# Kernel tuning notes

Measured on AMD Instinct MI355X. Metric: run time of the kernel, lower is better.

The kernel has to match this reference:

```python
import jax, jax.numpy as jnp
import numpy as np

EPS = 1e-5
KS = 3
PAD = 1


def _bn(x, g, b, m, v):
    inv = g / jnp.sqrt(v + EPS)
    return x * inv[None, :, None, None] + (b - m * inv)[None, :, None, None]


def _deform_conv2d(x, off_w, off_b, w):
    # x: (B,C,H,W); off_w: (2*9,C,3,3); w: (Cout,C,3,3)
    B, C, H, W = x.shape
    N = KS * KS
    off = jax.lax.conv_general_dilated(x, off_w, (1, 1), ((PAD, PAD), (PAD, PAD)))
    off = off + off_b[None, :, None, None]                      # (B,2N,H,W)
    xp = jnp.pad(x, ((0, 0), (0, 0), (PAD, PAD), (PAD, PAD)))
    Hp, Wp = H + 2 * PAD, W + 2 * PAD
    r = jnp.arange(KS, dtype=x.dtype) - (KS - 1) // 2           # kernel offsets
    pny = jnp.repeat(r, KS)                                     # row-major (dy)
    pnx = jnp.tile(r, KS)                                       # row-major (dx)
    p0y = jnp.arange(1, H + 1, dtype=x.dtype)[None, None, :, None]
    p0x = jnp.arange(1, W + 1, dtype=x.dtype)[None, None, None, :]
    py = off[:, :N] + pny[None, :, None, None] + p0y            # (B,N,H,W)
    px = off[:, N:] + pnx[None, :, None, None] + p0x
    py = jnp.clip(py, 0.0, Hp - 1.0)
    px = jnp.clip(px, 0.0, Wp - 1.0)
    fy = jax.lax.stop_gradient(jnp.floor(py))                   # indices detached (as in torch impl)
    fx = jax.lax.stop_gradient(jnp.floor(px))
    qy0 = jnp.clip(fy, 0.0, Hp - 1.0)
    qx0 = jnp.clip(fx, 0.0, Wp - 1.0)
    qy1 = jnp.clip(fy + 1.0, 0.0, Hp - 1.0)
    qx1 = jnp.clip(fx + 1.0, 0.0, Wp - 1.0)
    xf = xp.reshape(B, C, Hp * Wp)

    def gather(qy, qx):
        idx = (qy * Wp + qx).astype(jnp.int32)                  # (B,N,H,W)
        return jax.vmap(lambda m_, i_: m_[:, i_])(xf, idx)       # (B,C,N,H,W)

    g_lt = (1.0 + (qy0 - py)) * (1.0 + (qx0 - px))
    g_rb = (1.0 - (qy1 - py)) * (1.0 - (qx1 - px))
    g_lb = (1.0 + (qy0 - py)) * (1.0 - (qx1 - px))
    g_rt = (1.0 - (qy1 - py)) * (1.0 + (qx0 - px))
    xo = (g_lt[:, None] * gather(qy0, qx0) + g_rb[:, None] * gather(qy1, qx1)
          + g_lb[:, None] * gather(qy0, qx1) + g_rt[:, None] * gather(qy1, qx0))
    # (B,C,N,H,W) -> (B,C,H*KS,W*KS): N = (row, col) row-major
    xo = xo.reshape(B, C, KS, KS, H, W).transpose(0, 1, 4, 2, 5, 3).reshape(B, C, H * KS, W * KS)
    return jax.lax.conv_general_dilated(xo, w, (KS, KS), 'VALID')


def _forward(x, dc1_offw, dc1_offb, dc1_w, bn1_g, bn1_b, bn1_m, bn1_v,
             dc2_offw, dc2_offb, dc2_w, bn2_g, bn2_b, bn2_m, bn2_v,
             id_w, id_b, bn3_g, bn3_b, bn3_m, bn3_v):
    h = jax.nn.relu(_bn(_deform_conv2d(x, dc1_offw, dc1_offb, dc1_w), bn1_g, bn1_b, bn1_m, bn1_v))
    h = _bn(_deform_conv2d(h, dc2_offw, dc2_offb, dc2_w), bn2_g, bn2_b, bn2_m, bn2_v)
    idt = jnp.einsum('bchw,oc->bohw', x, id_w[:, :, 0, 0]) + id_b[None, :, None, None]
    idt = _bn(idt, bn3_g, bn3_b, bn3_m, bn3_v)
    return jax.nn.relu(h + idt)


def setup_inputs() -> dict:
    key = jax.random.key(0)
    ks = jax.random.split(key, 16)
    B, Cin, Cout, H, W = 2, 64, 128, 128, 128
    N2 = 2 * KS * KS
    d = {}
    d['x'] = jax.random.normal(ks[0], (B, Cin, H, W), jnp.float32)
    d['dc1_offw'] = jax.random.normal(ks[1], (N2, Cin, KS, KS), jnp.float32) * 0.01
    d['dc1_offb'] = jnp.zeros((N2,), jnp.float32)
    d['dc1_w'] = jax.random.normal(ks[2], (Cout, Cin, KS, KS), jnp.float32) * 0.05
    d['bn1_g'] = 1.0 + 0.1 * jax.random.normal(ks[3], (Cout,), jnp.float32)
    d['bn1_b'] = 0.1 * jax.random.normal(ks[4], (Cout,), jnp.float32)
    d['bn1_m'] = 0.1 * jax.random.normal(ks[5], (Cout,), jnp.float32)
    d['bn1_v'] = jnp.ones((Cout,), jnp.float32)
    d['dc2_offw'] = jax.random.normal(ks[6], (N2, Cout, KS, KS), jnp.float32) * 0.01
    d['dc2_offb'] = jnp.zeros((N2,), jnp.float32)
    d['dc2_w'] = jax.random.normal(ks[7], (Cout, Cout, KS, KS), jnp.float32) * 0.03
    d['bn2_g'] = 1.0 + 0.1 * jax.random.normal(ks[8], (Cout,), jnp.float32)
    d['bn2_b'] = 0.1 * jax.random.normal(ks[9], (Cout,), jnp.float32)
    d['bn2_m'] = 0.1 * jax.random.normal(ks[10], (Cout,), jnp.float32)
    d['bn2_v'] = jnp.ones((Cout,), jnp.float32)
    d['id_w'] = jax.random.normal(ks[11], (Cout, Cin, 1, 1), jnp.float32) * 0.1
    d['id_b'] = jnp.zeros((Cout,), jnp.float32)
    d['bn3_g'] = 1.0 + 0.1 * jax.random.normal(ks[12], (Cout,), jnp.float32)
    d['bn3_b'] = 0.1 * jax.random.normal(ks[13], (Cout,), jnp.float32)
    d['bn3_m'] = 0.1 * jax.random.normal(ks[14], (Cout,), jnp.float32)
    d['bn3_v'] = jnp.ones((Cout,), jnp.float32)
    return d


def reference(x, dc1_offw, dc1_offb, dc1_w, bn1_g, bn1_b, bn1_m, bn1_v,
              dc2_offw, dc2_offb, dc2_w, bn2_g, bn2_b, bn2_m, bn2_v,
              id_w, id_b, bn3_g, bn3_b, bn3_m, bn3_v):
    return _forward(x, dc1_offw, dc1_offb, dc1_w, bn1_g, bn1_b, bn1_m, bn1_v,
                    dc2_offw, dc2_offb, dc2_w, bn2_g, bn2_b, bn2_m, bn2_v,
                    id_w, id_b, bn3_g, bn3_b, bn3_m, bn3_v)
```

## Files before the change

kernel.cpp:

```cpp
#include <hip/hip_runtime.h>
#include <math.h>

#define HH 128
#define WW 128
#define HWSZ (HH * WW)
#define BB 2
#define COUT 128

typedef __bf16 bf16x8 __attribute__((ext_vector_type(8)));
typedef float f32x4 __attribute__((ext_vector_type(4)));
typedef float f32x2 __attribute__((ext_vector_type(2)));
typedef short s16x8 __attribute__((ext_vector_type(8)));
typedef short s16x4 __attribute__((ext_vector_type(4)));
typedef unsigned short u16x4 __attribute__((ext_vector_type(4)));
typedef unsigned short u16x8 __attribute__((ext_vector_type(8)));

__device__ __forceinline__ short tobf(float f) {
  union { float f; unsigned u; } v; v.f = f;
  unsigned r = v.u + 0x7fffu + ((v.u >> 16) & 1u);
  return (short)(r >> 16);
}
__device__ __forceinline__ float asf(unsigned u) {
  union { unsigned u; float f; } v; v.u = u;
  return v.f;
}
__device__ __forceinline__ f32x2 up2(unsigned u) {
  f32x2 r; r[0] = asf(u << 16); r[1] = asf(u & 0xffff0000u); return r;
}
__device__ __forceinline__ unsigned trunc2bf(f32x2 v) {
  union { float f; unsigned u; } a, b;
  a.f = v[0]; b.f = v[1];
  return __builtin_amdgcn_perm(b.u, a.u, 0x07060302u);
}

#define PA0 73728
#define PA1 221184
#define PA2 229376
#define PA3 247808
#define PA4 284672
#define PA5 284928
__global__ __launch_bounds__(256) void prep_all_kernel(
    const float* __restrict__ dc1_w, const float* __restrict__ dc2_w,
    const float* __restrict__ id_w, const float* __restrict__ dc1_offw,
    const float* __restrict__ dc2_offw,
    const float* g1, const float* b1, const float* m1, const float* v1,
    const float* g2, const float* b2, const float* m2, const float* v2,
    const float* g3, const float* b3, const float* m3, const float* v3,
    const float* idb,
    short* __restrict__ wbf1, short* __restrict__ wbf2,
    short* __restrict__ woff1, short* __restrict__ woff2,
    float* __restrict__ cb1, float* __restrict__ cb2) {
  int idx = blockIdx.x * 256 + threadIdx.x;
  if (idx < PA0) {
    int o = idx / 576, k = idx - o * 576;
    float inv = g1[o] / sqrtf(v1[o] + 1e-5f);
    int col = (k % 9) * 64 + k / 9;
    int di = (((col >> 5) * 2 + (o >> 6)) * 4 + ((o >> 4) & 3)) * 512
           + (((o & 15) | (((col >> 3) & 3) << 4)) * 8) + (col & 7);
    wbf1[di] = tobf(dc1_w[(size_t)o * 576 + k] * inv);
  } else if (idx < PA1) {
    int j = idx - PA0;
    int o = j / 1152, k = j - o * 1152;
    float inv = g2[o] / sqrtf(v2[o] + 1e-5f);
    int col = (k % 9) * 128 + k / 9;
    int di = (((col >> 5) * 2 + (o >> 6)) * 4 + ((o >> 4) & 3)) * 512
           + (((o & 15) | (((col >> 3) & 3) << 4)) * 8) + (col & 7);
    wbf2[di] = tobf(dc2_w[(size_t)o * 1152 + k] * inv);
  } else if (idx < PA2) {
    int j = idx - PA1;
    int o = j >> 6, k = j & 63;
    float inv = g3[o] / sqrtf(v3[o] + 1e-5f);
    int col = 1152 + k;
    int di = (((col >> 5) * 2 + (o >> 6)) * 4 + ((o >> 4) & 3)) * 512
           + (((o & 15) | (((col >> 3) & 3) << 4)) * 8) + (col & 7);
    wbf2[di] = tobf(id_w[(size_t)o * 64 + k] * inv);
  } else if (idx < PA3) {
    int j = idx - PA2;
    int o = j / 576, k = j - o * 576;
    int col = (k % 9) * 64 + k / 9;
    int di = ((col >> 5) * 2 + (o >> 4)) * 512 + ((col >> 3) & 3) * 128
           + (o & 15) * 8 + (col & 7);
    woff1[di] = (o < 18) ? tobf(dc1_offw[(size_t)o * 576 + k]) : (short)0;
  } else if (idx < PA4) {
    int j = idx - PA3;
    int o = j / 1152, k = j - o * 1152;
    int col = (k % 9) * 128 + k / 9;
    int di = ((col >> 5) * 2 + (o >> 4)) * 512 + ((col >> 3) & 3) * 128
           + (o & 15) * 8 + (col & 7);
    woff2[di] = (o < 18) ? tobf(dc2_offw[(size_t)o * 1152 + k]) : (short)0;
  } else if (idx < PA5) {
    int j = idx - PA4;
    if (j < 128) {
      float inv = g1[j] / sqrtf(v1[j] + 1e-5f);
      cb1[j] = b1[j] - m1[j] * inv;
    } else {
      int o = j - 128;
      float inv2_ = g2[o] / sqrtf(v2[o] + 1e-5f);
      float inv3_ = g3[o] / sqrtf(v3[o] + 1e-5f);
      cb2[o] = (b2[o] - m2[o] * inv2_) + idb[o] * inv3_ + (b3[o] - m3[o] * inv3_);
    }
  }
}

__global__ __launch_bounds__(256) void xcast_kernel(const float* __restrict__ x,
                                                    unsigned short* __restrict__ xn) {
  __shared__ short lds[64 * 72];
  int tid = threadIdx.x;
  int gp0 = blockIdx.x * 64;
  int b = gp0 >> 14;
  int pl0 = gp0 & 16383;
  int p = tid & 63;
  int cb = (tid >> 6) * 16;
#pragma unroll
  for (int i = 0; i < 16; i++) {
    int c = cb + i;
    lds[p * 72 + c] = tobf(x[((size_t)(b * 64 + c)) * HWSZ + pl0 + p]);
  }
  __syncthreads();
  int pw = tid >> 2, cseg = (tid & 3) * 16;
  u16x8 a = *(const u16x8*)&lds[pw * 72 + cseg];
  u16x8 b8 = *(const u16x8*)&lds[pw * 72 + cseg + 8];
  *(u16x8*)&xn[(size_t)(gp0 + pw) * 64 + cseg] = a;
  *(u16x8*)&xn[(size_t)(gp0 + pw) * 64 + cseg + 8] = b8;
}

template <int CSH>
__global__ __launch_bounds__(512, 4) void offconv_mfma_kernel(
    const unsigned short* __restrict__ in, const short* __restrict__ woff,
    const float* __restrict__ offb, float* __restrict__ off) {
  __shared__ float redf[4 * 64 * 8];
  constexpr int Cin = 1 << CSH;
  constexpr int HK = (9 << CSH) >> 1;
  constexpr int NCh = HK >> 5;
  const int tid = threadIdx.x;
  const int lane = tid & 63, wv = tid >> 6;
  const int pxg = wv & 3, kh = wv >> 2;
  const int pb = ((blockIdx.x & 7) << 6) | (blockIdx.x >> 3);
  const int pix0 = pb << 6;
  const int x0 = pix0 & 127, y = (pix0 >> 7) & 127, b = pix0 >> 14;
  const unsigned short* inb = in + (size_t)b * HWSZ * Cin;
  const int l15 = lane & 15, quad = lane >> 4;
  const int px = x0 + pxg * 16 + l15;

  f32x4 acc[2];
  acc[0] = (f32x4){0.f, 0.f, 0.f, 0.f};
  acc[1] = (f32x4){0.f, 0.f, 0.f, 0.f};

#pragma unroll
  for (int i = 0; i < NCh; i++) {
    int k0 = kh * HK + i * 32;
    int n = k0 >> CSH;
    int c0 = (k0 & (Cin - 1)) + quad * 8;
    int yy = y + n / 3 - 1;
    int xx = px + n % 3 - 1;
    bf16x8 bv = {};
    if (((unsigned)yy < (unsigned)HH) && ((unsigned)xx < (unsigned)WW))
      bv = *(const bf16x8*)&inb[((size_t)yy * WW + xx) * Cin + c0];
    int fbase = (k0 >> 5) * 1024 + lane * 8;
    bf16x8 a0 = *(const bf16x8*)&woff[fbase];
    bf16x8 a1 = *(const bf16x8*)&woff[fbase + 512];
    acc[0] = __builtin_amdgcn_mfma_f32_16x16x32_bf16(a0, bv, acc[0], 0, 0, 0);
    acc[1] = __builtin_amdgcn_mfma_f32_16x16x32_bf16(a1, bv, acc[1], 0, 0, 0);
  }
  if (kh == 1) {
    *(f32x4*)&redf[(pxg * 64 + lane) * 8] = acc[0];
    *(f32x4*)&redf[(pxg * 64 + lane) * 8 + 4] = acc[1];
  }
  __syncthreads();
  if (kh == 0) {
    acc[0] += *(const f32x4*)&redf[(pxg * 64 + lane) * 8];
    acc[1] += *(const f32x4*)&redf[(pxg * 64 + lane) * 8 + 4];
#pragma unroll
    for (int ot = 0; ot < 2; ot++) {
#pragma unroll
      for (int r = 0; r < 4; r++) {
        int o = ot * 16 + quad * 4 + r;
        if (o < 18)
          off[(size_t)(b * 18 + o) * HWSZ + y * WW + px] = acc[ot][r] + offb[o];
      }
    }
  }
}

#define LOADW(P, kc_)                                           \
  {                                                             \
    const short* wf_ = wfb + (size_t)(kc_) * 4096;              \
    P##w0 = *(const bf16x8*)(wf_);                              \
    P##w1 = *(const bf16x8*)(wf_ + 512);                        \
    P##w2 = *(const bf16x8*)(wf_ + 1024);                       \
    P##w3 = *(const bf16x8*)(wf_ + 1536);                       \
    P##w4 = *(const bf16x8*)(wf_ + 2048);                       \
    P##w5 = *(const bf16x8*)(wf_ + 2560);                       \
    P##w6 = *(const bf16x8*)(wf_ + 3072);                       \
    P##w7 = *(const bf16x8*)(wf_ + 3584);                       \
  }

#define LOADT(P, kc_)                                           \
  {                                                             \
    int k0_ = (kc_) << 5;                                       \
    int n_ = k0_ >> CSH;                                        \
    int c0_ = (k0_ & (Cin - 1)) + cq * 8;                       \
    uint4 d4_ = dsu[(n_ << 5) + dp];                            \
    int dx_ = (int)(d4_.w & 0xffffu);                           \
    int dy_ = (int)d4_.w >> 16;                                 \
    const unsigned short* ptr_ = inb + (int)d4_.z + c0_;        \
    P##q0 = *(const uint4*)(ptr_);                              \
    P##q1 = *(const uint4*)(ptr_ + dx_);                        \
    P##q2 = *(const uint4*)(ptr_ + dy_);                        \
    P##q3 = *(const uint4*)(ptr_ + dx_ + dy_);                  \
    P##wa = d4_.x;                                              \
    P##wb = d4_.y;                                              \
  }

#define COMPUTE(P)                                                            \
  {                                                                           \
    float w0_ = asf(P##wa << 16), w1_ = asf(P##wa & 0xffff0000u);             \
    float w2_ = asf(P##wb << 16), w3_ = asf(P##wb & 0xffff0000u);             \
    f32x2 v0_ = up2(P##q0.x) * w0_ + up2(P##q1.x) * w1_                       \
              + up2(P##q2.x) * w2_ + up2(P##q3.x) * w3_;                      \
    f32x2 v1_ = up2(P##q0.y) * w0_ + up2(P##q1.y) * w1_                       \
              + up2(P##q2.y) * w2_ + up2(P##q3.y) * w3_;                      \
    f32x2 v2_ = up2(P##q0.z) * w0_ + up2(P##q1.z) * w1_                       \
              + up2(P##q2.z) * w2_ + up2(P##q3.z) * w3_;                      \
    f32x2 v3_ = up2(P##q0.w) * w0_ + up2(P##q1.w) * w1_                       \
              + up2(P##q2.w) * w2_ + up2(P##q3.w) * w3_;                      \
    union { int i[4]; bf16x8 v; } bu_;                                        \
    bu_.i[0] = __builtin_amdgcn_ds_bpermute(baddr, (int)trunc2bf(v0_));       \
    bu_.i[1] = __builtin_amdgcn_ds_bpermute(baddr, (int)trunc2bf(v1_));       \
    bu_.i[2] = __builtin_amdgcn_ds_bpermute(baddr, (int)trunc2bf(v2_));       \
    bu_.i[3] = __builtin_amdgcn_ds_bpermute(baddr, (int)trunc2bf(v3_));       \
    bf16x8 bfr_ = bu_.v;                                                      \
    acc[0] = __builtin_amdgcn_mfma_f32_16x16x32_bf16(P##w0, bfr_, acc[0], 0, 0, 0); \
    acc[1] = __builtin_amdgcn_mfma_f32_16x16x32_bf16(P##w1, bfr_, acc[1], 0, 0, 0); \
    acc[2] = __builtin_amdgcn_mfma_f32_16x16x32_bf16(P##w2, bfr_, acc[2], 0, 0, 0); \
    acc[3] = __builtin_amdgcn_mfma_f32_16x16x32_bf16(P##w3, bfr_, acc[3], 0, 0, 0); \
    acc[4] = __builtin_amdgcn_mfma_f32_16x16x32_bf16(P##w4, bfr_, acc[4], 0, 0, 0); \
    acc[5] = __builtin_amdgcn_mfma_f32_16x16x32_bf16(P##w5, bfr_, acc[5], 0, 0, 0); \
    acc[6] = __builtin_amdgcn_mfma_f32_16x16x32_bf16(P##w6, bfr_, acc[6], 0, 0, 0); \
    acc[7] = __builtin_amdgcn_mfma_f32_16x16x32_bf16(P##w7, bfr_, acc[7], 0, 0, 0); \
  }

template <int CSH, int KCONV, int KTOT, int MODE>
__global__ __launch_bounds__(256, 3) void deform_mfma_kernel(
    const unsigned short* __restrict__ in, const float* __restrict__ off,
    const short* __restrict__ wbf, const float* __restrict__ cbv,
    const unsigned short* __restrict__ xid, float* __restrict__ outf,
    unsigned short* __restrict__ outb) {
  __shared__ __align__(16) char smem[25088];
  uint4* dsu = (uint4*)smem;
  f32x4* redf = (f32x4*)smem;
  short* trans = (short*)(smem + 16384);

  const int tid = threadIdx.x;
  const int lane = tid & 63, wv = tid >> 6;
  const int pb = ((blockIdx.x & 7) << 7) | (blockIdx.x >> 3);
  const int pix0 = pb << 5;
  const int x0 = pix0 & 127, y = (pix0 >> 7) & 127, b = pix0 >> 14;
  constexpr int Cin = 1 << CSH;
  const unsigned short* inb = in + (size_t)b * HWSZ * Cin;
  const int l15 = lane & 15, quad = lane >> 4;
  const int pxg = wv & 1, kh = wv >> 1;
  const int dp = pxg * 16 + (lane >> 2);
  const int cq = lane & 3;
  const int baddr = (((lane & 15) << 2) | (lane >> 4)) << 2;

  constexpr int NC = KTOT >> 5;
  constexpr int NCONV = KCONV >> 5;
  constexpr int HC = NC >> 1;
  const int kcBeg = kh * HC;
  const int kcEnd = kcBeg + HC;
  const int kcEndConv = (kcEnd < NCONV) ? kcEnd : NCONV;
  const short* wfb = wbf + lane * 8;

  bf16x8 Aw0, Aw1, Aw2, Aw3, Aw4, Aw5, Aw6, Aw7;
  bf16x8 Bw0, Bw1, Bw2, Bw3, Bw4, Bw5, Bw6, Bw7;
  uint4 Aq0, Aq1, Aq2, Aq3, Bq0, Bq1, Bq2, Bq3;
  unsigned Awa, Awb, Bwa, Bwb;

  LOADW(A, kcBeg);

  for (int t = tid; t < 288; t += 256) {
    int n = t >> 5, pp = t & 31;
    float offy = off[(size_t)(b * 18 + n) * HWSZ + y * WW + x0 + pp];
    float offx = off[(size_t)(b * 18 + 9 + n) * HWSZ + y * WW + x0 + pp];
    float py = offy + (float)(n / 3 - 1) + (float)(y + 1);
    float px = offx + (float)(n % 3 - 1) + (float)(x0 + pp + 1);
    py = fminf(fmaxf(py, 0.f), 129.f);
    px = fminf(fmaxf(px, 0.f), 129.f);
    float fy = floorf(py), fx = floorf(px);
    float qy1 = fminf(fy + 1.f, 129.f), qx1 = fminf(fx + 1.f, 129.f);
    float ty0 = 1.f + fy - py, ty1 = 1.f - (qy1 - py);
    float tx0 = 1.f + fx - px, tx1 = 1.f - (qx1 - px);
    int iy0 = (int)fy - 1, ix0 = (int)fx - 1;
    int iy1 = (int)qy1 - 1, ix1 = (int)qx1 - 1;
    if ((unsigned)iy0 >= (unsigned)HH) ty0 = 0.f;
    if ((unsigned)iy1 >= (unsigned)HH) ty1 = 0.f;
    if ((unsigned)ix0 >= (unsigned)WW) tx0 = 0.f;
    if ((unsigned)ix1 >= (unsigned)WW) tx1 = 0.f;
    int by0 = min(max(iy0, 0), HH - 1), by1 = min(max(iy1, 0), HH - 1);
    int bx0 = min(max(ix0, 0), WW - 1), bx1 = min(max(ix1, 0), WW - 1);
    uint4 d4;
    d4.x = (unsigned)(unsigned short)tobf(ty0 * tx0)
         | ((unsigned)(unsigned short)tobf(ty0 * tx1) << 16);
    d4.y = (unsigned)(unsigned short)tobf(ty1 * tx0)
         | ((unsigned)(unsigned short)tobf(ty1 * tx1) << 16);
    d4.z = (unsigned)((by0 * WW + bx0) * Cin);
    d4.w = (unsigned)((((by1 - by0) * WW * Cin) << 16) | ((bx1 - bx0) * Cin));
    dsu[t] = d4;
  }

  f32x4 acc[8];
#pragma unroll
  for (int j = 0; j < 8; j++) acc[j] = (f32x4){0.f, 0.f, 0.f, 0.f};

  __syncthreads();

  LOADT(A, kcBeg);
  int i = kcBeg;
  for (; i + 2 <= kcEndConv; i += 2) {
    LOADW(B, i + 1);
    LOADT(B, i + 1);
    COMPUTE(A);
    if (i + 2 < kcEndConv) {
      LOADW(A, i + 2);
      LOADT(A, i + 2);
    }
    COMPUTE(B);
  }
  if (i < kcEndConv) {
    COMPUTE(A);
    i++;
  }

  if (KCONV < KTOT) {
    for (; i < kcEnd; i++) {
      LOADW(A, i);
      int c = ((i << 5) - KCONV) + cq * 8;
      uint4 pk = *(const uint4*)&xid[((size_t)(b * HWSZ) + y * WW + x0 + dp) * 64 + c];
      union { int i[4]; bf16x8 v; } bu;
      bu.i[0] = __builtin_amdgcn_ds_bpermute(baddr, (int)pk.x);
      bu.i[1] = __builtin_amdgcn_ds_bpermute(baddr, (int)pk.y);
      bu.i[2] = __builtin_amdgcn_ds_bpermute(baddr, (int)pk.z);
      bu.i[3] = __builtin_amdgcn_ds_bpermute(baddr, (int)pk.w);
      bf16x8 bfr = bu.v;
      acc[0] = __builtin_amdgcn_mfma_f32_16x16x32_bf16(Aw0, bfr, acc[0], 0, 0, 0);
      acc[1] = __builtin_amdgcn_mfma_f32_16x16x32_bf16(Aw1, bfr, acc[1], 0, 0, 0);
      acc[2] = __builtin_amdgcn_mfma_f32_16x16x32_bf16(Aw2, bfr, acc[2], 0, 0, 0);
      acc[3] = __builtin_amdgcn_mfma_f32_16x16x32_bf16(Aw3, bfr, acc[3], 0, 0, 0);
      acc[4] = __builtin_amdgcn_mfma_f32_16x16x32_bf16(Aw4, bfr, acc[4], 0, 0, 0);
      acc[5] = __builtin_amdgcn_mfma_f32_16x16x32_bf16(Aw5, bfr, acc[5], 0, 0, 0);
      acc[6] = __builtin_amdgcn_mfma_f32_16x16x32_bf16(Aw6, bfr, acc[6], 0, 0, 0);
      acc[7] = __builtin_amdgcn_mfma_f32_16x16x32_bf16(Aw7, bfr, acc[7], 0, 0, 0);
    }
  }

  __syncthreads();
  if (kh == 1) {
#pragma unroll
    for (int f = 0; f < 8; f++) redf[f * 128 + pxg * 64 + lane] = acc[f];
  }
  __syncthreads();
  if (kh == 0) {
#pragma unroll
    for (int f = 0; f < 8; f++) acc[f] += redf[f * 128 + pxg * 64 + lane];
    if (MODE == 1) {
#pragma unroll
      for (int f = 0; f < 8; f++) {
#pragma unroll
        for (int r = 0; r < 4; r++) {
          int o = (f >> 2) * 64 + (f & 3) * 16 + quad * 4 + r;
          outf[(size_t)(b * COUT + o) * HWSZ + y * WW + x0 + pxg * 16 + l15] =
              fmaxf(acc[f][r] + cbv[o], 0.f);
        }
      }
    } else {
      int pl = pxg * 16 + l15;
#pragma unroll
      for (int f = 0; f < 8; f++) {
        s16x4 t4;
#pragma unroll
        for (int r = 0; r < 4; r++) {
          int o = (f >> 2) * 64 + (f & 3) * 16 + quad * 4 + r;
          t4[r] = tobf(fmaxf(acc[f][r] + cbv[o], 0.f));
        }
        *(s16x4*)&trans[pl * 136 + (f >> 2) * 64 + (f & 3) * 16 + quad * 4] = t4;
      }
    }
  }
  if (MODE == 0) {
    __syncthreads();
    int pw = tid >> 3, cs = (tid & 7) * 16;
    u16x8 va = *(const u16x8*)&trans[pw * 136 + cs];
    u16x8 vb = *(const u16x8*)&trans[pw * 136 + cs + 8];
    size_t gb = ((size_t)(b * HWSZ) + y * WW + x0 + pw) * 128 + cs;
    *(u16x8*)&outb[gb] = va;
    *(u16x8*)&outb[gb + 8] = vb;
  }
}

extern "C" void kernel_launch(void* const* d_in, const int* in_sizes, int n_in,
                              void* d_out, int out_size, void* d_ws, size_t ws_size,
                              hipStream_t stream) {
  const float* x        = (const float*)d_in[0];
  const float* dc1_offw = (const float*)d_in[1];
  const float* dc1_offb = (const float*)d_in[2];
  const float* dc1_w    = (const float*)d_in[3];
  const float* bn1_g    = (const float*)d_in[4];
  const float* bn1_b    = (const float*)d_in[5];
  const float* bn1_m    = (const float*)d_in[6];
  const float* bn1_v    = (const float*)d_in[7];
  const float* dc2_offw = (const float*)d_in[8];
  const float* dc2_offb = (const float*)d_in[9];
  const float* dc2_w    = (const float*)d_in[10];
  const float* bn2_g    = (const float*)d_in[11];
  const float* bn2_b    = (const float*)d_in[12];
  const float* bn2_m    = (const float*)d_in[13];
  const float* bn2_v    = (const float*)d_in[14];
  const float* id_w     = (const float*)d_in[15];
  const float* id_b     = (const float*)d_in[16];
  const float* bn3_g    = (const float*)d_in[17];
  const float* bn3_b    = (const float*)d_in[18];
  const float* bn3_m    = (const float*)d_in[19];
  const float* bn3_v    = (const float*)d_in[20];

  float* wsf = (float*)d_ws;
  float* off1 = wsf;
  float* off2 = off1 + (size_t)BB * 18 * HWSZ;
  float* cb1  = off2 + (size_t)BB * 18 * HWSZ;
  float* cb2  = cb1 + 128;
  unsigned short* xbf = (unsigned short*)(cb2 + 128);
  unsigned short* h1  = xbf + (size_t)BB * HWSZ * 64;
  short* wbf1  = (short*)(h1 + (size_t)BB * HWSZ * COUT);
  short* wbf2  = wbf1 + (size_t)128 * 576;
  short* woff1 = wbf2 + (size_t)128 * 1216;
  short* woff2 = woff1 + (size_t)18 * 1024;

  hipLaunchKernelGGL(prep_all_kernel, dim3((PA5 + 255) / 256), dim3(256), 0, stream,
                     dc1_w, dc2_w, id_w, dc1_offw, dc2_offw,
                     bn1_g, bn1_b, bn1_m, bn1_v, bn2_g, bn2_b, bn2_m, bn2_v,
                     bn3_g, bn3_b, bn3_m, bn3_v, id_b,
                     wbf1, wbf2, woff1, woff2, cb1, cb2);
  hipLaunchKernelGGL(xcast_kernel, dim3(BB * HWSZ / 64), dim3(256), 0, stream, x, xbf);

  hipLaunchKernelGGL((offconv_mfma_kernel<6>), dim3(512), dim3(512), 0, stream,
                     xbf, woff1, dc1_offb, off1);
  hipLaunchKernelGGL((deform_mfma_kernel<6, 576, 576, 0>), dim3(1024), dim3(256), 0, stream,
                     xbf, off1, wbf1, cb1, (const unsigned short*)nullptr,
                     (float*)nullptr, h1);
  hipLaunchKernelGGL((offconv_mfma_kernel<7>), dim3(512), dim3(512), 0, stream,
                     h1, woff2, dc2_offb, off2);
  hipLaunchKernelGGL((deform_mfma_kernel<7, 1152, 1216, 1>), dim3(1024), dim3(256), 0, stream,
                     h1, off2, wbf2, cb2, xbf, (float*)d_out,
                     (unsigned short*)nullptr);
}
```

Measured before the change: 182.5 us.

## Double pixel tile per block to reuse weight fragments across two MFMA B-tiles

Each deform conv block now covers 64 pixels instead of 32, and each wave blends two 16-pixel groups so every loaded weight fragment feeds two MFMAs. Launch grids are halved and the shared memory for sampling descriptors, reduction and transpose doubles. The aim is to halve weight-load traffic per output. The cost is more registers (16 accumulators, twice the gather registers), launch bounds relaxed from 3 to 2 blocks per CU, and fewer blocks overall.

```diff
diff --git a/kernel.cpp b/kernel.cpp
--- a/kernel.cpp
+++ b/kernel.cpp
@@ -200,67 +200,105 @@
     int k0_ = (kc_) << 5;                                       \
     int n_ = k0_ >> CSH;                                        \
     int c0_ = (k0_ & (Cin - 1)) + cq * 8;                       \
-    uint4 d4_ = dsu[(n_ << 5) + dp];                            \
+    uint4 d4_ = dsu[(n_ << 6) + dp0];                           \
     int dx_ = (int)(d4_.w & 0xffffu);                           \
     int dy_ = (int)d4_.w >> 16;                                 \
-    const unsigned short* ptr_ = inb + (int)d4_.z + c0_;        \
-    P##q0 = *(const uint4*)(ptr_);                              \
-    P##q1 = *(const uint4*)(ptr_ + dx_);                        \
-    P##q2 = *(const uint4*)(ptr_ + dy_);                        \
-    P##q3 = *(const uint4*)(ptr_ + dx_ + dy_);                  \
-    P##wa = d4_.x;                                              \
-    P##wb = d4_.y;                                              \
+    const unsigned short* p_ = inb + (int)d4_.z + c0_;          \
+    P##q00 = *(const uint4*)(p_);                               \
+    P##q01 = *(const uint4*)(p_ + dx_);                         \
+    P##q02 = *(const uint4*)(p_ + dy_);                         \
+    P##q03 = *(const uint4*)(p_ + dx_ + dy_);                   \
+    P##wa0 = d4_.x; P##wb0 = d4_.y;                             \
+    uint4 e4_ = dsu[(n_ << 6) + dp1];                           \
+    int ex_ = (int)(e4_.w & 0xffffu);                           \
+    int ey_ = (int)e4_.w >> 16;                                 \
+    const unsigned short* q_ = inb + (int)e4_.z + c0_;          \
+    P##q10 = *(const uint4*)(q_);                               \
+    P##q11 = *(const uint4*)(q_ + ex_);                         \
+    P##q12 = *(const uint4*)(q_ + ey_);                         \
+    P##q13 = *(const uint4*)(q_ + ex_ + ey_);                   \
+    P##wa1 = e4_.x; P##wb1 = e4_.y;                             \
+  }
+
+#define BLEND1(r0, r1, r2, r3, wav, wbv, pkv)                                 \
+  {                                                                           \
+    float w0_ = asf((wav) << 16), w1_ = asf((wav) & 0xffff0000u);             \
+    float w2_ = asf((wbv) << 16), w3_ = asf((wbv) & 0xffff0000u);             \
+    f32x2 v0_ = up2(r0.x) * w0_ + up2(r1.x) * w1_                             \
+              + up2(r2.x) * w2_ + up2(r3.x) * w3_;                            \
+    f32x2 v1_ = up2(r0.y) * w0_ + up2(r1.y) * w1_                             \
+              + up2(r2.y) * w2_ + up2(r3.y) * w3_;                            \
+    f32x2 v2_ = up2(r0.z) * w0_ + up2(r1.z) * w1_                             \
+              + up2(r2.z) * w2_ + up2(r3.z) * w3_;                            \
+    f32x2 v3_ = up2(r0.w) * w0_ + up2(r1.w) * w1_                             \
+              + up2(r2.w) * w2_ + up2(r3.w) * w3_;                            \
+    pkv.x = trunc2bf(v0_); pkv.y = trunc2bf(v1_);                             \
+    pkv.z = trunc2bf(v2_); pkv.w = trunc2bf(v3_);                             \
+  }
+
+#define XPOSE(pkv, bfrv)                                                      \
+  {                                                                           \
+    union { int i[4]; bf16x8 v; } bu_;                                        \
+    bu_.i[0] = __builtin_amdgcn_ds_bpermute(baddr, (int)pkv.x);               \
+    bu_.i[1] = __builtin_amdgcn_ds_bpermute(baddr, (int)pkv.y);               \
+    bu_.i[2] = __builtin_amdgcn_ds_bpermute(baddr, (int)pkv.z);               \
+    bu_.i[3] = __builtin_amdgcn_ds_bpermute(baddr, (int)pkv.w);               \
+    bfrv = bu_.v;                                                             \
+  }
+
+#define MFMA16(P, bfr0v, bfr1v)                                                     \
+  {                                                                                 \
+    acc[0] = __builtin_amdgcn_mfma_f32_16x16x32_bf16(P##w0, bfr0v, acc[0], 0, 0, 0);  \
+    acc[8] = __builtin_amdgcn_mfma_f32_16x16x32_bf16(P##w0, bfr1v, acc[8], 0, 0, 0);  \
+    acc[1] = __builtin_amdgcn_mfma_f32_16x16x32_bf16(P##w1, bfr0v, acc[1], 0, 0, 0);  \
+    acc[9] = __builtin_amdgcn_mfma_f32_16x16x32_bf16(P##w1, bfr1v, acc[9], 0, 0, 0);  \
+    acc[2] = __builtin_amdgcn_mfma_f32_16x16x32_bf16(P##w2, bfr0v, acc[2], 0, 0, 0);  \
+    acc[10] = __builtin_amdgcn_mfma_f32_16x16x32_bf16(P##w2, bfr1v, acc[10], 0, 0, 0);\
+    acc[3] = __builtin_amdgcn_mfma_f32_16x16x32_bf16(P##w3, bfr0v, acc[3], 0, 0, 0);  \
+    acc[11] = __builtin_amdgcn_mfma_f32_16x16x32_bf16(P##w3, bfr1v, acc[11], 0, 0, 0);\
+    acc[4] = __builtin_amdgcn_mfma_f32_16x16x32_bf16(P##w4, bfr0v, acc[4], 0, 0, 0);  \
+    acc[12] = __builtin_amdgcn_mfma_f32_16x16x32_bf16(P##w4, bfr1v, acc[12], 0, 0, 0);\
+    acc[5] = __builtin_amdgcn_mfma_f32_16x16x32_bf16(P##w5, bfr0v, acc[5], 0, 0, 0);  \
+    acc[13] = __builtin_amdgcn_mfma_f32_16x16x32_bf16(P##w5, bfr1v, acc[13], 0, 0, 0);\
+    acc[6] = __builtin_amdgcn_mfma_f32_16x16x32_bf16(P##w6, bfr0v, acc[6], 0, 0, 0);  \
+    acc[14] = __builtin_amdgcn_mfma_f32_16x16x32_bf16(P##w6, bfr1v, acc[14], 0, 0, 0);\
+    acc[7] = __builtin_amdgcn_mfma_f32_16x16x32_bf16(P##w7, bfr0v, acc[7], 0, 0, 0);  \
+    acc[15] = __builtin_amdgcn_mfma_f32_16x16x32_bf16(P##w7, bfr1v, acc[15], 0, 0, 0);\
   }
 
 #define COMPUTE(P)                                                            \
   {                                                                           \
-    float w0_ = asf(P##wa << 16), w1_ = asf(P##wa & 0xffff0000u);             \
-    float w2_ = asf(P##wb << 16), w3_ = asf(P##wb & 0xffff0000u);             \
-    f32x2 v0_ = up2(P##q0.x) * w0_ + up2(P##q1.x) * w1_                       \
-              + up2(P##q2.x) * w2_ + up2(P##q3.x) * w3_;                      \
-    f32x2 v1_ = up2(P##q0.y) * w0_ + up2(P##q1.y) * w1_                       \
-              + up2(P##q2.y) * w2_ + up2(P##q3.y) * w3_;                      \
-    f32x2 v2_ = up2(P##q0.z) * w0_ + up2(P##q1.z) * w1_                       \
-              + up2(P##q2.z) * w2_ + up2(P##q3.z) * w3_;                      \
-    f32x2 v3_ = up2(P##q0.w) * w0_ + up2(P##q1.w) * w1_                       \
-              + up2(P##q2.w) * w2_ + up2(P##q3.w) * w3_;                      \
-    union { int i[4]; bf16x8 v; } bu_;                                        \
-    bu_.i[0] = __builtin_amdgcn_ds_bpermute(baddr, (int)trunc2bf(v0_));       \
-    bu_.i[1] = __builtin_amdgcn_ds_bpermute(baddr, (int)trunc2bf(v1_));       \
-    bu_.i[2] = __builtin_amdgcn_ds_bpermute(baddr, (int)trunc2bf(v2_));       \
-    bu_.i[3] = __builtin_amdgcn_ds_bpermute(baddr, (int)trunc2bf(v3_));       \
-    bf16x8 bfr_ = bu_.v;                                                      \
-    acc[0] = __builtin_amdgcn_mfma_f32_16x16x32_bf16(P##w0, bfr_, acc[0], 0, 0, 0); \
-    acc[1] = __builtin_amdgcn_mfma_f32_16x16x32_bf16(P##w1, bfr_, acc[1], 0, 0, 0); \
-    acc[2] = __builtin_amdgcn_mfma_f32_16x16x32_bf16(P##w2, bfr_, acc[2], 0, 0, 0); \
-    acc[3] = __builtin_amdgcn_mfma_f32_16x16x32_bf16(P##w3, bfr_, acc[3], 0, 0, 0); \
-    acc[4] = __builtin_amdgcn_mfma_f32_16x16x32_bf16(P##w4, bfr_, acc[4], 0, 0, 0); \
-    acc[5] = __builtin_amdgcn_mfma_f32_16x16x32_bf16(P##w5, bfr_, acc[5], 0, 0, 0); \
-    acc[6] = __builtin_amdgcn_mfma_f32_16x16x32_bf16(P##w6, bfr_, acc[6], 0, 0, 0); \
-    acc[7] = __builtin_amdgcn_mfma_f32_16x16x32_bf16(P##w7, bfr_, acc[7], 0, 0, 0); \
+    uint4 pk0_, pk1_;                                                         \
+    BLEND1(P##q00, P##q01, P##q02, P##q03, P##wa0, P##wb0, pk0_);             \
+    BLEND1(P##q10, P##q11, P##q12, P##q13, P##wa1, P##wb1, pk1_);             \
+    bf16x8 bf0_, bf1_;                                                        \
+    XPOSE(pk0_, bf0_);                                                        \
+    XPOSE(pk1_, bf1_);                                                        \
+    MFMA16(P, bf0_, bf1_);                                                    \
   }
 
 template <int CSH, int KCONV, int KTOT, int MODE>
-__global__ __launch_bounds__(256, 3) void deform_mfma_kernel(
+__global__ __launch_bounds__(256, 2) void deform_mfma_kernel(
     const unsigned short* __restrict__ in, const float* __restrict__ off,
     const short* __restrict__ wbf, const float* __restrict__ cbv,
     const unsigned short* __restrict__ xid, float* __restrict__ outf,
     unsigned short* __restrict__ outb) {
-  __shared__ __align__(16) char smem[25088];
+  __shared__ __align__(16) char smem[50176];
   uint4* dsu = (uint4*)smem;
   f32x4* redf = (f32x4*)smem;
-  short* trans = (short*)(smem + 16384);
+  short* trans = (short*)(smem + 32768);
 
   const int tid = threadIdx.x;
   const int lane = tid & 63, wv = tid >> 6;
-  const int pb = ((blockIdx.x & 7) << 7) | (blockIdx.x >> 3);
-  const int pix0 = pb << 5;
+  const int pb = ((blockIdx.x & 7) << 6) | (blockIdx.x >> 3);
+  const int pix0 = pb << 6;
   const int x0 = pix0 & 127, y = (pix0 >> 7) & 127, b = pix0 >> 14;
   constexpr int Cin = 1 << CSH;
   const unsigned short* inb = in + (size_t)b * HWSZ * Cin;
   const int l15 = lane & 15, quad = lane >> 4;
   const int pxg = wv & 1, kh = wv >> 1;
-  const int dp = pxg * 16 + (lane >> 2);
+  const int dp0 = pxg * 32 + (lane >> 2);
+  const int dp1 = dp0 + 16;
   const int cq = lane & 3;
   const int baddr = (((lane & 15) << 2) | (lane >> 4)) << 2;
 
@@ -274,13 +312,14 @@
 
   bf16x8 Aw0, Aw1, Aw2, Aw3, Aw4, Aw5, Aw6, Aw7;
   bf16x8 Bw0, Bw1, Bw2, Bw3, Bw4, Bw5, Bw6, Bw7;
-  uint4 Aq0, Aq1, Aq2, Aq3, Bq0, Bq1, Bq2, Bq3;
-  unsigned Awa, Awb, Bwa, Bwb;
+  uint4 Aq00, Aq01, Aq02, Aq03, Aq10, Aq11, Aq12, Aq13;
+  uint4 Bq00, Bq01, Bq02, Bq03, Bq10, Bq11, Bq12, Bq13;
+  unsigned Awa0, Awb0, Awa1, Awb1, Bwa0, Bwb0, Bwa1, Bwb1;
 
   LOADW(A, kcBeg);
 
-  for (int t = tid; t < 288; t += 256) {
-    int n = t >> 5, pp = t & 31;
+  for (int t = tid; t < 576; t += 256) {
+    int n = t >> 6, pp = t & 63;
     float offy = off[(size_t)(b * 18 + n) * HWSZ + y * WW + x0 + pp];
     float offx = off[(size_t)(b * 18 + 9 + n) * HWSZ + y * WW + x0 + pp];
     float py = offy + (float)(n / 3 - 1) + (float)(y + 1);
@@ -309,9 +348,9 @@
     dsu[t] = d4;
   }
 
-  f32x4 acc[8];
-#pragma unroll
-  for (int j = 0; j < 8; j++) acc[j] = (f32x4){0.f, 0.f, 0.f, 0.f};
+  f32x4 acc[16];
+#pragma unroll
+  for (int j = 0; j < 16; j++) acc[j] = (f32x4){0.f, 0.f, 0.f, 0.f};
 
   __syncthreads();
 
@@ -336,65 +375,60 @@
     for (; i < kcEnd; i++) {
       LOADW(A, i);
       int c = ((i << 5) - KCONV) + cq * 8;
-      uint4 pk = *(const uint4*)&xid[((size_t)(b * HWSZ) + y * WW + x0 + dp) * 64 + c];
-      union { int i[4]; bf16x8 v; } bu;
-      bu.i[0] = __builtin_amdgcn_ds_bpermute(baddr, (int)pk.x);
-      bu.i[1] = __builtin_amdgcn_ds_bpermute(baddr, (int)pk.y);
-      bu.i[2] = __builtin_amdgcn_ds_bpermute(baddr, (int)pk.z);
-      bu.i[3] = __builtin_amdgcn_ds_bpermute(baddr, (int)pk.w);
-      bf16x8 bfr = bu.v;
-      acc[0] = __builtin_amdgcn_mfma_f32_16x16x32_bf16(Aw0, bfr, acc[0], 0, 0, 0);
-      acc[1] = __builtin_amdgcn_mfma_f32_16x16x32_bf16(Aw1, bfr, acc[1], 0, 0, 0);
-      acc[2] = __builtin_amdgcn_mfma_f32_16x16x32_bf16(Aw2, bfr, acc[2], 0, 0, 0);
-      acc[3] = __builtin_amdgcn_mfma_f32_16x16x32_bf16(Aw3, bfr, acc[3], 0, 0, 0);
-      acc[4] = __builtin_amdgcn_mfma_f32_16x16x32_bf16(Aw4, bfr, acc[4], 0, 0, 0);
-      acc[5] = __builtin_amdgcn_mfma_f32_16x16x32_bf16(Aw5, bfr, acc[5], 0, 0, 0);
-      acc[6] = __builtin_amdgcn_mfma_f32_16x16x32_bf16(Aw6, bfr, acc[6], 0, 0, 0);
-      acc[7] = __builtin_amdgcn_mfma_f32_16x16x32_bf16(Aw7, bfr, acc[7], 0, 0, 0);
+      uint4 pk0 = *(const uint4*)&xid[((size_t)(b * HWSZ) + y * WW + x0 + dp0) * 64 + c];
+      uint4 pk1 = *(const uint4*)&xid[((size_t)(b * HWSZ) + y * WW + x0 + dp1) * 64 + c];
+      bf16x8 bf0, bf1;
+      XPOSE(pk0, bf0);
+      XPOSE(pk1, bf1);
+      MFMA16(A, bf0, bf1);
     }
   }
 
   __syncthreads();
   if (kh == 1) {
 #pragma unroll
-    for (int f = 0; f < 8; f++) redf[f * 128 + pxg * 64 + lane] = acc[f];
+    for (int f = 0; f < 16; f++) redf[f * 128 + pxg * 64 + lane] = acc[f];
   }
   __syncthreads();
   if (kh == 0) {
 #pragma unroll
-    for (int f = 0; f < 8; f++) acc[f] += redf[f * 128 + pxg * 64 + lane];
+    for (int f = 0; f < 16; f++) acc[f] += redf[f * 128 + pxg * 64 + lane];
     if (MODE == 1) {
 #pragma unroll
-      for (int f = 0; f < 8; f++) {
+      for (int f = 0; f < 16; f++) {
+        int px_ = x0 + pxg * 32 + (f >> 3) * 16 + l15;
+        int fo = f & 7;
 #pragma unroll
         for (int r = 0; r < 4; r++) {
-          int o = (f >> 2) * 64 + (f & 3) * 16 + quad * 4 + r;
-          outf[(size_t)(b * COUT + o) * HWSZ + y * WW + x0 + pxg * 16 + l15] =
+          int o = (fo >> 2) * 64 + (fo & 3) * 16 + quad * 4 + r;
+          outf[(size_t)(b * COUT + o) * HWSZ + y * WW + px_] =
               fmaxf(acc[f][r] + cbv[o], 0.f);
         }
       }
     } else {
-      int pl = pxg * 16 + l15;
-#pragma unroll
-      for (int f = 0; f < 8; f++) {
+#pragma unroll
+      for (int f = 0; f < 16; f++) {
+        int pl = pxg * 32 + (f >> 3) * 16 + l15;
+        int fo = f & 7;
         s16x4 t4;
 #pragma unroll
         for (int r = 0; r < 4; r++) {
-          int o = (f >> 2) * 64 + (f & 3) * 16 + quad * 4 + r;
+          int o = (fo >> 2) * 64 + (fo & 3) * 16 + quad * 4 + r;
           t4[r] = tobf(fmaxf(acc[f][r] + cbv[o], 0.f));
         }
-        *(s16x4*)&trans[pl * 136 + (f >> 2) * 64 + (f & 3) * 16 + quad * 4] = t4;
+        *(s16x4*)&trans[pl * 136 + (fo >> 2) * 64 + (fo & 3) * 16 + quad * 4] = t4;
       }
     }
   }
   if (MODE == 0) {
     __syncthreads();
-    int pw = tid >> 3, cs = (tid & 7) * 16;
-    u16x8 va = *(const u16x8*)&trans[pw * 136 + cs];
-    u16x8 vb = *(const u16x8*)&trans[pw * 136 + cs + 8];
+    int pw = tid >> 2, cs = (tid & 3) * 32;
     size_t gb = ((size_t)(b * HWSZ) + y * WW + x0 + pw) * 128 + cs;
-    *(u16x8*)&outb[gb] = va;
-    *(u16x8*)&outb[gb + 8] = vb;
+#pragma unroll
+    for (int s = 0; s < 4; s++) {
+      u16x8 v8 = *(const u16x8*)&trans[pw * 136 + cs + s * 8];
+      *(u16x8*)&outb[gb + s * 8] = v8;
+    }
   }
 }
 
@@ -444,12 +478,12 @@
 
   hipLaunchKernelGGL((offconv_mfma_kernel<6>), dim3(512), dim3(512), 0, stream,
                      xbf, woff1, dc1_offb, off1);
-  hipLaunchKernelGGL((deform_mfma_kernel<6, 576, 576, 0>), dim3(1024), dim3(256), 0, stream,
+  hipLaunchKernelGGL((deform_mfma_kernel<6, 576, 576, 0>), dim3(512), dim3(256), 0, stream,
                      xbf, off1, wbf1, cb1, (const unsigned short*)nullptr,
                      (float*)nullptr, h1);
   hipLaunchKernelGGL((offconv_mfma_kernel<7>), dim3(512), dim3(512), 0, stream,
                      h1, woff2, dc2_offb, off2);
-  hipLaunchKernelGGL((deform_mfma_kernel<7, 1152, 1216, 1>), dim3(1024), dim3(256), 0, stream,
+  hipLaunchKernelGGL((deform_mfma_kernel<7, 1152, 1216, 1>), dim3(512), dim3(256), 0, stream,
                      h1, off2, wbf2, cb2, xbf, (float*)d_out,
                      (unsigned short*)nullptr);
 }
```

Result: faster. 178.0 us (-2.4%).
